# Optimization experiments

Hardware: AMD Instinct MI355X
Metric: run time of the kernel (lower is better)

## Reference

```python
import jax, jax.numpy as jnp
import numpy as np

HID_X = 64
MLP_RATIO = 4
EPS_NORM = 1e-12  # F.normalize default eps
EPS_RMS = 1e-6


def _l2norm_dim2(w):
    # normalize along dim=-2 (the input-feature axis of each per-sample matrix)
    n = jnp.sqrt(jnp.sum(w * w, axis=-2, keepdims=True))
    return w / jnp.maximum(n, EPS_NORM)


def setup_inputs() -> dict:
    key = jax.random.key(0)
    k1, k2, k3, k4 = jax.random.split(key, 4)
    B, N, D, S = 64, 4096, HID_X, 1024
    total = 3 * D * D * MLP_RATIO
    x = jax.random.normal(k1, (B, N, D), dtype=jnp.float32)
    s = jax.random.normal(k2, (B, S), dtype=jnp.float32)
    W_pg = jax.random.normal(k3, (S, total), dtype=jnp.float32) * 0.02
    b_pg = jax.random.normal(k4, (total,), dtype=jnp.float32) * 0.01
    scale = jnp.ones((D,), dtype=jnp.float32)
    return {"x": x, "s": s, "W_pg": W_pg, "b_pg": b_pg, "scale": scale}


def reference(x, s, W_pg, b_pg, scale):
    B, N, D = x.shape
    H = D * MLP_RATIO
    # hypernetwork: generate per-sample MLP weights
    mlp_params = s @ W_pg + b_pg  # [B, 3*D*H]
    g_p, v_p, f_p = jnp.split(mlp_params, 3, axis=-1)
    fc1_gate = _l2norm_dim2(g_p.reshape(B, D, H))
    fc1_value = _l2norm_dim2(v_p.reshape(B, D, H))
    fc2 = _l2norm_dim2(f_p.reshape(B, H, D))
    # RMSNorm (eps=1e-6)
    rrms = jax.lax.rsqrt(jnp.mean(x * x, axis=-1, keepdims=True) + EPS_RMS)
    xn = x * rrms * scale
    gate = jnp.einsum('bnd,bdh->bnh', xn, fc1_gate)
    value = jnp.einsum('bnd,bdh->bnh', xn, fc1_value)
    h = jax.nn.silu(gate) * value
    out = jnp.einsum('bnh,bhd->bnd', h, fc2) + x
    return out
```

## Files before the change

kernel.cpp:

```cpp
#include <hip/hip_runtime.h>
#include <hip/hip_bf16.h>

#define BB 64
#define NN 4096
#define DD 64
#define HH 256
#define SS 1024
#define TOTAL 49152
#define MAT_ELEMS 16384

typedef __bf16 bf16x8 __attribute__((ext_vector_type(8)));
typedef float  f32x4  __attribute__((ext_vector_type(4)));

__global__ __launch_bounds__(256, 4) void k1_gemm(
    const float* __restrict__ s, const float* __restrict__ W,
    const float* __restrict__ bias, float* __restrict__ params)
{
    const int n0 = blockIdx.x * 64;
    const int t  = threadIdx.x;
    const int tx = t & 15, ty = t >> 4;

    __shared__ float sA[64 * 36];
    __shared__ float sB[32 * 68];

    float acc[4][4] = {};

    const float* sp0 = &s[(size_t)(t >> 3) * SS + (t & 7) * 4];
    const float* sp1 = sp0 + (size_t)32 * SS;
    const float* wp0 = &W[(size_t)(t >> 4) * TOTAL + n0 + (t & 15) * 4];
    const float* wp1 = wp0 + (size_t)16 * TOTAL;

    float4 pA0 = *(const float4*)(sp0);
    float4 pA1 = *(const float4*)(sp1);
    float4 pB0 = *(const float4*)(wp0);
    float4 pB1 = *(const float4*)(wp1);

    for (int k0 = 0; k0 < SS; k0 += 32) {
        *(float4*)&sA[(t >> 3) * 36 + (t & 7) * 4]        = pA0;
        *(float4*)&sA[((t >> 3) + 32) * 36 + (t & 7) * 4] = pA1;
        *(float4*)&sB[(t >> 4) * 68 + (t & 15) * 4]        = pB0;
        *(float4*)&sB[((t >> 4) + 16) * 68 + (t & 15) * 4] = pB1;
        __syncthreads();
        if (k0 + 32 < SS) {
            pA0 = *(const float4*)(sp0 + k0 + 32);
            pA1 = *(const float4*)(sp1 + k0 + 32);
            pB0 = *(const float4*)(wp0 + (size_t)(k0 + 32) * TOTAL);
            pB1 = *(const float4*)(wp1 + (size_t)(k0 + 32) * TOTAL);
        }
        #pragma unroll
        for (int kk = 0; kk < 32; kk++) {
            float4 b = *(const float4*)&sB[kk * 68 + tx * 4];
            float a0 = sA[(ty * 4 + 0) * 36 + kk];
            float a1 = sA[(ty * 4 + 1) * 36 + kk];
            float a2 = sA[(ty * 4 + 2) * 36 + kk];
            float a3 = sA[(ty * 4 + 3) * 36 + kk];
            acc[0][0] += a0 * b.x; acc[0][1] += a0 * b.y; acc[0][2] += a0 * b.z; acc[0][3] += a0 * b.w;
            acc[1][0] += a1 * b.x; acc[1][1] += a1 * b.y; acc[1][2] += a1 * b.z; acc[1][3] += a1 * b.w;
            acc[2][0] += a2 * b.x; acc[2][1] += a2 * b.y; acc[2][2] += a2 * b.z; acc[2][3] += a2 * b.w;
            acc[3][0] += a3 * b.x; acc[3][1] += a3 * b.y; acc[3][2] += a3 * b.z; acc[3][3] += a3 * b.w;
        }
        __syncthreads();
    }

    #pragma unroll
    for (int r = 0; r < 4; r++) {
        int m = ty * 4 + r;
        int n = n0 + tx * 4;
        float4 bv = *(const float4*)&bias[n];
        float4 o;
        o.x = acc[r][0] + bv.x; o.y = acc[r][1] + bv.y;
        o.z = acc[r][2] + bv.z; o.w = acc[r][3] + bv.w;
        *(float4*)&params[(size_t)m * TOTAL + n] = o;
    }
}

__global__ __launch_bounds__(256) void k2_fc1(
    const float* __restrict__ params, __bf16* __restrict__ WgT, __bf16* __restrict__ WvT)
{
    const int b   = blockIdx.x >> 2;
    const int mat = (blockIdx.x >> 1) & 1;
    const int hh  = blockIdx.x & 1;
    const int t   = threadIdx.x;
    __shared__ float sh[64 * 130];
    __shared__ float rnorm[128];

    const float* src = params + (size_t)b * TOTAL + mat * MAT_ELEMS + hh * 128;
    #pragma unroll
    for (int i = 0; i < 32; i++) {
        int idx = t + i * 256;
        int d = idx >> 7, h = idx & 127;
        sh[d * 130 + h] = src[d * 256 + h];
    }
    __syncthreads();
    if (t < 128) {
        float sum = 0.f;
        #pragma unroll
        for (int d = 0; d < 64; d++) {
            float v = sh[d * 130 + t];
            sum += v * v;
        }
        rnorm[t] = 1.0f / fmaxf(sqrtf(sum), 1e-12f);
    }
    __syncthreads();
    __bf16* dst = (mat ? WvT : WgT) + (size_t)b * MAT_ELEMS;
    #pragma unroll
    for (int i = 0; i < 32; i++) {
        int idx = t + i * 256;
        int hl = idx >> 6, d = idx & 63;
        dst[(hh * 128 + hl) * 64 + d] = (__bf16)(sh[d * 130 + hl] * rnorm[hl]);
    }
}

__global__ __launch_bounds__(256) void k2_fc2(
    const float* __restrict__ params, __bf16* __restrict__ WfT)
{
    const int b  = blockIdx.x >> 1;
    const int dh = blockIdx.x & 1;
    const int t  = threadIdx.x;
    __shared__ float sh[256 * 33];
    __shared__ float psum[8 * 32];
    __shared__ float rnorm[32];

    const float* src = params + (size_t)b * TOTAL + 2 * MAT_ELEMS + dh * 32;
    #pragma unroll
    for (int i = 0; i < 32; i++) {
        int idx = t + i * 256;
        int h = idx >> 5, d = idx & 31;
        sh[h * 33 + d] = src[h * 64 + d];
    }
    __syncthreads();
    {
        int d = t & 31, seg = t >> 5;
        float sum = 0.f;
        #pragma unroll
        for (int hi = 0; hi < 32; hi++) {
            float v = sh[(seg * 32 + hi) * 33 + d];
            sum += v * v;
        }
        psum[seg * 32 + d] = sum;
    }
    __syncthreads();
    if (t < 32) {
        float sum = 0.f;
        #pragma unroll
        for (int seg = 0; seg < 8; seg++) sum += psum[seg * 32 + t];
        rnorm[t] = 1.0f / fmaxf(sqrtf(sum), 1e-12f);
    }
    __syncthreads();
    __bf16* dst = WfT + (size_t)b * MAT_ELEMS;
    #pragma unroll
    for (int i = 0; i < 32; i++) {
        int idx = t + i * 256;
        int d = idx >> 8, h = idx & 255;
        dst[(dh * 32 + d) * 256 + h] = (__bf16)(sh[h * 33 + d] * rnorm[d]);
    }
}

__global__ __launch_bounds__(256, 4) void k3_fused(
    const float* __restrict__ x, const float* __restrict__ scale,
    const __bf16* __restrict__ WgT, const __bf16* __restrict__ WvT,
    const __bf16* __restrict__ WfT, float* __restrict__ out)
{
    const int b    = blockIdx.x >> 5;
    const int rb   = blockIdx.x & 31;
    const int t    = threadIdx.x;
    const int w    = t >> 6;
    const int lane = t & 63;
    const int l15  = lane & 15;
    const int quad = lane >> 4;

    __shared__ __bf16 h_sh[4 * 32 * 136];

    const size_t row_base = ((size_t)b * NN + rb * 128) * DD;

    float sc[16];
    *(float4*)&sc[0]  = *(const float4*)&scale[quad * 8];
    *(float4*)&sc[4]  = *(const float4*)&scale[quad * 8 + 4];
    *(float4*)&sc[8]  = *(const float4*)&scale[32 + quad * 8];
    *(float4*)&sc[12] = *(const float4*)&scale[32 + quad * 8 + 4];

    bf16x8 afrag[2][2];
    #pragma unroll
    for (int mt = 0; mt < 2; mt++) {
        int row = w * 32 + mt * 16 + l15;
        const float* xp = &x[row_base + (size_t)row * DD + quad * 8];
        float v[16];
        *(float4*)&v[0]  = *(const float4*)(xp);
        *(float4*)&v[4]  = *(const float4*)(xp + 4);
        *(float4*)&v[8]  = *(const float4*)(xp + 32);
        *(float4*)&v[12] = *(const float4*)(xp + 36);
        float ss = 0.f;
        #pragma unroll
        for (int j = 0; j < 16; j++) ss += v[j] * v[j];
        ss += __shfl_xor(ss, 16, 64);
        ss += __shfl_xor(ss, 32, 64);
        float rr = rsqrtf(ss * (1.0f / 64.0f) + 1e-6f);
        #pragma unroll
        for (int j = 0; j < 8; j++) {
            afrag[mt][0][j] = (__bf16)(v[j] * rr * sc[j]);
            afrag[mt][1][j] = (__bf16)(v[8 + j] * rr * sc[8 + j]);
        }
    }

    f32x4 oacc[2][4] = {};
    const __bf16* wg_b = WgT + (size_t)b * MAT_ELEMS;
    const __bf16* wv_b = WvT + (size_t)b * MAT_ELEMS;
    const __bf16* wf_b = WfT + (size_t)b * MAT_ELEMS;
    __bf16* hbuf = &h_sh[w * 32 * 136];

    for (int half = 0; half < 2; half++) {
        #pragma unroll
        for (int npl = 0; npl < 4; npl++) {
            const int np = half * 4 + npl;
            bf16x8 bg[2][2], bv[2][2];
            #pragma unroll
            for (int sub = 0; sub < 2; sub++) {
                int nt = np * 2 + sub;
                const __bf16* gp = &wg_b[(nt * 16 + l15) * 64 + quad * 8];
                const __bf16* vp = &wv_b[(nt * 16 + l15) * 64 + quad * 8];
                bg[sub][0] = *(const bf16x8*)(gp);
                bg[sub][1] = *(const bf16x8*)(gp + 32);
                bv[sub][0] = *(const bf16x8*)(vp);
                bv[sub][1] = *(const bf16x8*)(vp + 32);
            }
            #pragma unroll
            for (int sub = 0; sub < 2; sub++) {
                #pragma unroll
                for (int mt = 0; mt < 2; mt++) {
                    f32x4 g = {0.f, 0.f, 0.f, 0.f}, vv = {0.f, 0.f, 0.f, 0.f};
                    g  = __builtin_amdgcn_mfma_f32_16x16x32_bf16(afrag[mt][0], bg[sub][0], g, 0, 0, 0);
                    g  = __builtin_amdgcn_mfma_f32_16x16x32_bf16(afrag[mt][1], bg[sub][1], g, 0, 0, 0);
                    vv = __builtin_amdgcn_mfma_f32_16x16x32_bf16(afrag[mt][0], bv[sub][0], vv, 0, 0, 0);
                    vv = __builtin_amdgcn_mfma_f32_16x16x32_bf16(afrag[mt][1], bv[sub][1], vv, 0, 0, 0);
                    #pragma unroll
                    for (int r = 0; r < 4; r++) {
                        float gv = g[r];
                        float sig = __builtin_amdgcn_rcpf(1.0f + __expf(-gv));
                        float hval = gv * sig * vv[r];
                        hbuf[(mt * 16 + quad * 4 + r) * 136 + npl * 32 + sub * 16 + l15] = (__bf16)hval;
                    }
                }
            }
        }
        #pragma unroll
        for (int kpl = 0; kpl < 4; kpl++) {
            const int kp = half * 4 + kpl;
            bf16x8 bf[4];
            #pragma unroll
            for (int dt = 0; dt < 4; dt++)
                bf[dt] = *(const bf16x8*)&wf_b[(dt * 16 + l15) * 256 + kp * 32 + quad * 8];
            #pragma unroll
            for (int mt = 0; mt < 2; mt++) {
                bf16x8 ah = *(const bf16x8*)&hbuf[(mt * 16 + l15) * 136 + kpl * 32 + quad * 8];
                #pragma unroll
                for (int dt = 0; dt < 4; dt++)
                    oacc[mt][dt] = __builtin_amdgcn_mfma_f32_16x16x32_bf16(ah, bf[dt], oacc[mt][dt], 0, 0, 0);
            }
        }
    }

    #pragma unroll
    for (int mt = 0; mt < 2; mt++) {
        int r0 = w * 32 + mt * 16 + quad * 4;
        #pragma unroll
        for (int rg = 0; rg < 4; rg++) {
            size_t roff = row_base + (size_t)(r0 + rg) * DD;
            #pragma unroll
            for (int dt = 0; dt < 4; dt++) {
                int col = dt * 16 + l15;
                out[roff + col] = oacc[mt][dt][rg] + x[roff + col];
            }
        }
    }
}

extern "C" void kernel_launch(void* const* d_in, const int* in_sizes, int n_in,
                              void* d_out, int out_size, void* d_ws, size_t ws_size,
                              hipStream_t stream)
{
    const float* x     = (const float*)d_in[0];
    const float* s     = (const float*)d_in[1];
    const float* W_pg  = (const float*)d_in[2];
    const float* b_pg  = (const float*)d_in[3];
    const float* scale = (const float*)d_in[4];
    float* out = (float*)d_out;

    char* ws = (char*)d_ws;
    float*  params = (float*)ws;
    __bf16* WgT    = (__bf16*)(ws + 12582912);
    __bf16* WvT    = (__bf16*)(ws + 14680064);
    __bf16* WfT    = (__bf16*)(ws + 16777216);

    k1_gemm<<<TOTAL / 64, 256, 0, stream>>>(s, W_pg, b_pg, params);
    k2_fc1<<<BB * 4, 256, 0, stream>>>(params, WgT, WvT);
    k2_fc2<<<BB * 2, 256, 0, stream>>>(params, WfT);
    k3_fused<<<BB * 32, 256, 0, stream>>>(x, scale, WgT, WvT, WfT, out);
}
```

Before: 438.5 us.

## Split-K hypernetwork GEMM with larger 8x8 register tiles and fused reduction

```diff
diff --git a/kernel.cpp b/kernel.cpp
--- a/kernel.cpp
+++ b/kernel.cpp
@@ -8,152 +8,182 @@
 #define SS 1024
 #define TOTAL 49152
 #define MAT_ELEMS 16384
+#define PSLICE 3145728
 
 typedef __bf16 bf16x8 __attribute__((ext_vector_type(8)));
 typedef float  f32x4  __attribute__((ext_vector_type(4)));
 
-__global__ __launch_bounds__(256, 4) void k1_gemm(
+__global__ __launch_bounds__(256, 3) void k1_gemm(
     const float* __restrict__ s, const float* __restrict__ W,
-    const float* __restrict__ bias, float* __restrict__ params)
-{
-    const int n0 = blockIdx.x * 64;
+    float* __restrict__ partials)
+{
+    const int nb = blockIdx.x >> 2;
+    const int ks = blockIdx.x & 3;
+    const int n0 = nb * 256;
+    const int k0 = ks * 256;
     const int t  = threadIdx.x;
-    const int tx = t & 15, ty = t >> 4;
-
-    __shared__ float sA[64 * 36];
-    __shared__ float sB[32 * 68];
-
-    float acc[4][4] = {};
-
-    const float* sp0 = &s[(size_t)(t >> 3) * SS + (t & 7) * 4];
-    const float* sp1 = sp0 + (size_t)32 * SS;
-    const float* wp0 = &W[(size_t)(t >> 4) * TOTAL + n0 + (t & 15) * 4];
-    const float* wp1 = wp0 + (size_t)16 * TOTAL;
-
-    float4 pA0 = *(const float4*)(sp0);
-    float4 pA1 = *(const float4*)(sp1);
-    float4 pB0 = *(const float4*)(wp0);
-    float4 pB1 = *(const float4*)(wp1);
-
-    for (int k0 = 0; k0 < SS; k0 += 32) {
-        *(float4*)&sA[(t >> 3) * 36 + (t & 7) * 4]        = pA0;
-        *(float4*)&sA[((t >> 3) + 32) * 36 + (t & 7) * 4] = pA1;
-        *(float4*)&sB[(t >> 4) * 68 + (t & 15) * 4]        = pB0;
-        *(float4*)&sB[((t >> 4) + 16) * 68 + (t & 15) * 4] = pB1;
+    const int tx = t & 31;
+    const int ty = t >> 5;
+
+    __shared__ float sB[32 * 256];
+    __shared__ float sAT[32 * 68];
+
+    float acc[8][8] = {};
+
+    const int brow = t >> 3;
+    const int bcol = (t & 7) * 4;
+    const float* wp = &W[(size_t)(k0 + brow) * TOTAL + n0 + bcol];
+    const int am  = t >> 2;
+    const int akq = (t & 3) * 8;
+    const float* ap = &s[(size_t)am * SS + k0 + akq];
+
+    float4 pB[8];
+    #pragma unroll
+    for (int jj = 0; jj < 8; jj++) pB[jj] = *(const float4*)(wp + jj * 32);
+    float4 pA0 = *(const float4*)(ap);
+    float4 pA1 = *(const float4*)(ap + 4);
+
+    for (int st = 0; st < 8; st++) {
+        #pragma unroll
+        for (int jj = 0; jj < 8; jj++)
+            *(float4*)&sB[brow * 256 + bcol + jj * 32] = pB[jj];
+        sAT[(akq + 0) * 68 + am] = pA0.x;
+        sAT[(akq + 1) * 68 + am] = pA0.y;
+        sAT[(akq + 2) * 68 + am] = pA0.z;
+        sAT[(akq + 3) * 68 + am] = pA0.w;
+        sAT[(akq + 4) * 68 + am] = pA1.x;
+        sAT[(akq + 5) * 68 + am] = pA1.y;
+        sAT[(akq + 6) * 68 + am] = pA1.z;
+        sAT[(akq + 7) * 68 + am] = pA1.w;
         __syncthreads();
-        if (k0 + 32 < SS) {
-            pA0 = *(const float4*)(sp0 + k0 + 32);
-            pA1 = *(const float4*)(sp1 + k0 + 32);
-            pB0 = *(const float4*)(wp0 + (size_t)(k0 + 32) * TOTAL);
-            pB1 = *(const float4*)(wp1 + (size_t)(k0 + 32) * TOTAL);
-        }
-        #pragma unroll
+        if (st < 7) {
+            const float* wpn = wp + (size_t)(st + 1) * 32 * TOTAL;
+            #pragma unroll
+            for (int jj = 0; jj < 8; jj++) pB[jj] = *(const float4*)(wpn + jj * 32);
+            pA0 = *(const float4*)(ap + (st + 1) * 32);
+            pA1 = *(const float4*)(ap + (st + 1) * 32 + 4);
+        }
+        #pragma unroll 8
         for (int kk = 0; kk < 32; kk++) {
-            float4 b = *(const float4*)&sB[kk * 68 + tx * 4];
-            float a0 = sA[(ty * 4 + 0) * 36 + kk];
-            float a1 = sA[(ty * 4 + 1) * 36 + kk];
-            float a2 = sA[(ty * 4 + 2) * 36 + kk];
-            float a3 = sA[(ty * 4 + 3) * 36 + kk];
-            acc[0][0] += a0 * b.x; acc[0][1] += a0 * b.y; acc[0][2] += a0 * b.z; acc[0][3] += a0 * b.w;
-            acc[1][0] += a1 * b.x; acc[1][1] += a1 * b.y; acc[1][2] += a1 * b.z; acc[1][3] += a1 * b.w;
-            acc[2][0] += a2 * b.x; acc[2][1] += a2 * b.y; acc[2][2] += a2 * b.z; acc[2][3] += a2 * b.w;
-            acc[3][0] += a3 * b.x; acc[3][1] += a3 * b.y; acc[3][2] += a3 * b.z; acc[3][3] += a3 * b.w;
+            float4 b0 = *(const float4*)&sB[kk * 256 + tx * 8];
+            float4 b1 = *(const float4*)&sB[kk * 256 + tx * 8 + 4];
+            float4 a0 = *(const float4*)&sAT[kk * 68 + ty * 8];
+            float4 a1 = *(const float4*)&sAT[kk * 68 + ty * 8 + 4];
+            float av[8] = {a0.x, a0.y, a0.z, a0.w, a1.x, a1.y, a1.z, a1.w};
+            float bv[8] = {b0.x, b0.y, b0.z, b0.w, b1.x, b1.y, b1.z, b1.w};
+            #pragma unroll
+            for (int r = 0; r < 8; r++)
+                #pragma unroll
+                for (int c = 0; c < 8; c++)
+                    acc[r][c] += av[r] * bv[c];
         }
         __syncthreads();
     }
 
-    #pragma unroll
-    for (int r = 0; r < 4; r++) {
-        int m = ty * 4 + r;
-        int n = n0 + tx * 4;
-        float4 bv = *(const float4*)&bias[n];
-        float4 o;
-        o.x = acc[r][0] + bv.x; o.y = acc[r][1] + bv.y;
-        o.z = acc[r][2] + bv.z; o.w = acc[r][3] + bv.w;
-        *(float4*)&params[(size_t)m * TOTAL + n] = o;
+    float* pp = partials + (size_t)ks * PSLICE;
+    #pragma unroll
+    for (int r = 0; r < 8; r++) {
+        int m = ty * 8 + r;
+        float* o = pp + (size_t)m * TOTAL + n0 + tx * 8;
+        float4 o0 = {acc[r][0], acc[r][1], acc[r][2], acc[r][3]};
+        float4 o1 = {acc[r][4], acc[r][5], acc[r][6], acc[r][7]};
+        *(float4*)(o)     = o0;
+        *(float4*)(o + 4) = o1;
     }
 }
 
 __global__ __launch_bounds__(256) void k2_fc1(
-    const float* __restrict__ params, __bf16* __restrict__ WgT, __bf16* __restrict__ WvT)
-{
-    const int b   = blockIdx.x >> 2;
-    const int mat = (blockIdx.x >> 1) & 1;
-    const int hh  = blockIdx.x & 1;
-    const int t   = threadIdx.x;
-    __shared__ float sh[64 * 130];
-    __shared__ float rnorm[128];
-
-    const float* src = params + (size_t)b * TOTAL + mat * MAT_ELEMS + hh * 128;
-    #pragma unroll
-    for (int i = 0; i < 32; i++) {
-        int idx = t + i * 256;
-        int d = idx >> 7, h = idx & 127;
-        sh[d * 130 + h] = src[d * 256 + h];
-    }
-    __syncthreads();
-    if (t < 128) {
-        float sum = 0.f;
-        #pragma unroll
-        for (int d = 0; d < 64; d++) {
-            float v = sh[d * 130 + t];
-            sum += v * v;
-        }
-        rnorm[t] = 1.0f / fmaxf(sqrtf(sum), 1e-12f);
-    }
-    __syncthreads();
-    __bf16* dst = (mat ? WvT : WgT) + (size_t)b * MAT_ELEMS;
-    #pragma unroll
-    for (int i = 0; i < 32; i++) {
-        int idx = t + i * 256;
-        int hl = idx >> 6, d = idx & 63;
-        dst[(hh * 128 + hl) * 64 + d] = (__bf16)(sh[d * 130 + hl] * rnorm[hl]);
-    }
-}
-
-__global__ __launch_bounds__(256) void k2_fc2(
-    const float* __restrict__ params, __bf16* __restrict__ WfT)
-{
-    const int b  = blockIdx.x >> 1;
-    const int dh = blockIdx.x & 1;
-    const int t  = threadIdx.x;
-    __shared__ float sh[256 * 33];
+    const float* __restrict__ partials, const float* __restrict__ bias,
+    __bf16* __restrict__ WgT, __bf16* __restrict__ WvT)
+{
+    const int b    = blockIdx.x >> 4;
+    const int mat  = (blockIdx.x >> 3) & 1;
+    const int hg   = blockIdx.x & 7;
+    const int t    = threadIdx.x;
+    const int hh   = t & 31;
+    const int dseg = t >> 5;
+    const int h    = hg * 32 + hh;
+
     __shared__ float psum[8 * 32];
     __shared__ float rnorm[32];
 
-    const float* src = params + (size_t)b * TOTAL + 2 * MAT_ELEMS + dh * 32;
-    #pragma unroll
-    for (int i = 0; i < 32; i++) {
-        int idx = t + i * 256;
-        int h = idx >> 5, d = idx & 31;
-        sh[h * 33 + d] = src[h * 64 + d];
-    }
-    __syncthreads();
-    {
-        int d = t & 31, seg = t >> 5;
-        float sum = 0.f;
-        #pragma unroll
-        for (int hi = 0; hi < 32; hi++) {
-            float v = sh[(seg * 32 + hi) * 33 + d];
-            sum += v * v;
-        }
-        psum[seg * 32 + d] = sum;
-    }
+    const size_t base = (size_t)b * TOTAL + mat * MAT_ELEMS;
+    const float* p0 = partials + base;
+    const float* p1 = p0 + PSLICE;
+    const float* p2 = p1 + PSLICE;
+    const float* p3 = p2 + PSLICE;
+    const float* bi = bias + mat * MAT_ELEMS;
+
+    float val[8];
+    float ss = 0.f;
+    #pragma unroll
+    for (int j = 0; j < 8; j++) {
+        int off = (dseg * 8 + j) * 256 + h;
+        float v = p0[off] + p1[off] + p2[off] + p3[off] + bi[off];
+        val[j] = v;
+        ss += v * v;
+    }
+    psum[dseg * 32 + hh] = ss;
     __syncthreads();
     if (t < 32) {
-        float sum = 0.f;
-        #pragma unroll
-        for (int seg = 0; seg < 8; seg++) sum += psum[seg * 32 + t];
-        rnorm[t] = 1.0f / fmaxf(sqrtf(sum), 1e-12f);
+        float s2 = 0.f;
+        #pragma unroll
+        for (int g = 0; g < 8; g++) s2 += psum[g * 32 + t];
+        rnorm[t] = 1.0f / fmaxf(sqrtf(s2), 1e-12f);
     }
     __syncthreads();
-    __bf16* dst = WfT + (size_t)b * MAT_ELEMS;
-    #pragma unroll
-    for (int i = 0; i < 32; i++) {
-        int idx = t + i * 256;
-        int d = idx >> 8, h = idx & 255;
-        dst[(dh * 32 + d) * 256 + h] = (__bf16)(sh[h * 33 + d] * rnorm[d]);
-    }
+    float rn = rnorm[hh];
+    __bf16* dst = (mat ? WvT : WgT) + (size_t)b * MAT_ELEMS + (size_t)h * 64 + dseg * 8;
+    bf16x8 ov;
+    #pragma unroll
+    for (int j = 0; j < 8; j++) ov[j] = (__bf16)(val[j] * rn);
+    *(bf16x8*)dst = ov;
+}
+
+__global__ __launch_bounds__(256) void k2_fc2(
+    const float* __restrict__ partials, const float* __restrict__ bias,
+    __bf16* __restrict__ WfT)
+{
+    const int b    = blockIdx.x >> 3;
+    const int dg   = blockIdx.x & 7;
+    const int t    = threadIdx.x;
+    const int dd   = t & 7;
+    const int hseg = t >> 3;
+
+    __shared__ float psum[32 * 8];
+    __shared__ float rnorm[8];
+
+    const size_t base = (size_t)b * TOTAL + 2 * MAT_ELEMS;
+    const float* p0 = partials + base;
+    const float* p1 = p0 + PSLICE;
+    const float* p2 = p1 + PSLICE;
+    const float* p3 = p2 + PSLICE;
+    const float* bi = bias + 2 * MAT_ELEMS;
+
+    float val[8];
+    float ss = 0.f;
+    #pragma unroll
+    for (int j = 0; j < 8; j++) {
+        int off = (hseg * 8 + j) * 64 + dg * 8 + dd;
+        float v = p0[off] + p1[off] + p2[off] + p3[off] + bi[off];
+        val[j] = v;
+        ss += v * v;
+    }
+    psum[hseg * 8 + dd] = ss;
+    __syncthreads();
+    if (t < 8) {
+        float s2 = 0.f;
+        #pragma unroll
+        for (int g = 0; g < 32; g++) s2 += psum[g * 8 + t];
+        rnorm[t] = 1.0f / fmaxf(sqrtf(s2), 1e-12f);
+    }
+    __syncthreads();
+    float rn = rnorm[dd];
+    __bf16* dst = WfT + (size_t)b * MAT_ELEMS + (size_t)(dg * 8 + dd) * 256 + hseg * 8;
+    bf16x8 ov;
+    #pragma unroll
+    for (int j = 0; j < 8; j++) ov[j] = (__bf16)(val[j] * rn);
+    *(bf16x8*)dst = ov;
 }
 
 __global__ __launch_bounds__(256, 4) void k3_fused(
@@ -286,13 +316,13 @@
     float* out = (float*)d_out;
 
     char* ws = (char*)d_ws;
-    float*  params = (float*)ws;
-    __bf16* WgT    = (__bf16*)(ws + 12582912);
-    __bf16* WvT    = (__bf16*)(ws + 14680064);
-    __bf16* WfT    = (__bf16*)(ws + 16777216);
-
-    k1_gemm<<<TOTAL / 64, 256, 0, stream>>>(s, W_pg, b_pg, params);
-    k2_fc1<<<BB * 4, 256, 0, stream>>>(params, WgT, WvT);
-    k2_fc2<<<BB * 2, 256, 0, stream>>>(params, WfT);
+    float*  partials = (float*)ws;
+    __bf16* WgT      = (__bf16*)(ws + 50331648);
+    __bf16* WvT      = (__bf16*)(ws + 52428800);
+    __bf16* WfT      = (__bf16*)(ws + 54525952);
+
+    k1_gemm<<<768, 256, 0, stream>>>(s, W_pg, partials);
+    k2_fc1<<<BB * 16, 256, 0, stream>>>(partials, b_pg, WgT, WvT);
+    k2_fc2<<<BB * 8, 256, 0, stream>>>(partials, b_pg, WfT);
     k3_fused<<<BB * 32, 256, 0, stream>>>(x, scale, WgT, WvT, WfT, out);
 }
```

Result: slower. 497.8 us (+13.5%).
